# Kernel tuning notes

Measured on AMD Instinct MI355X. Metric: run time of the kernel, lower is better.

The kernel has to match this reference:

```python
import jax, jax.numpy as jnp
import numpy as np

N_NODES = 100000
N_EDGES = 1600000


def setup_inputs() -> dict:
    key = jax.random.key(0)
    ks = jax.random.split(key, 8)
    x = jax.random.normal(ks[0], (N_NODES, 128), dtype=jnp.float32)
    edge_index = jax.random.randint(ks[1], (2, N_EDGES), 0, N_NODES, dtype=jnp.int64)
    # Glorot-ish scaled weights per GCNConv defaults
    W1 = jax.random.normal(ks[2], (128, 64), dtype=jnp.float32) * (1.0 / np.sqrt(128))
    b1 = jnp.zeros((64,), dtype=jnp.float32)
    W2 = jax.random.normal(ks[3], (64, 64), dtype=jnp.float32) * (1.0 / np.sqrt(64))
    b2 = jnp.zeros((64,), dtype=jnp.float32)
    W3 = jax.random.normal(ks[4], (64, 32), dtype=jnp.float32) * (1.0 / np.sqrt(64))
    b3 = jnp.zeros((32,), dtype=jnp.float32)
    return {"x": x, "edge_index": edge_index, "W1": W1, "b1": b1,
            "W2": W2, "b2": b2, "W3": W3, "b3": b3}


def _gcn_norm(edge_index, n_nodes):
    # deg includes self-loop (+1); symmetric normalization D^-1/2 (A+I) D^-1/2
    dst = edge_index[1]
    deg = jax.ops.segment_sum(jnp.ones((edge_index.shape[1],), jnp.float32), dst,
                              num_segments=n_nodes) + 1.0
    dis = jnp.where(deg > 0, jax.lax.rsqrt(deg), 0.0)  # deg_inv_sqrt [N]
    return dis


def _gcn_conv(x, W, b, src, dst, dis, n_nodes):
    h = x @ W                                   # [N, out]
    coef = (dis[src] * dis[dst])[:, None]       # edge norm [E, 1]
    out = jax.ops.segment_sum(h[src] * coef, dst, num_segments=n_nodes)
    out = out + h * (dis * dis)[:, None]        # self-loop contribution
    return out + b


def reference(x, edge_index, W1, b1, W2, b2, W3, b3):
    n = x.shape[0]
    src, dst = edge_index[0], edge_index[1]
    dis = _gcn_norm(edge_index, n)
    h = _gcn_conv(x, W1, b1, src, dst, dis, n)
    h = jax.nn.relu(h)
    h = _gcn_conv(h, W2, b2, src, dst, dis, n)
    h = jax.nn.relu(h)
    h = _gcn_conv(h, W3, b3, src, dst, dis, n)
    return h
```

## Files before the change

kernel.cpp:

```cpp
#include <hip/hip_runtime.h>

#define N_NODES 100000
#define N_EDGES 1600000
#define NB ((N_NODES + 255) >> 8)


__global__ __launch_bounds__(256) void k_bhist(const int* __restrict__ dst,
                                               int* __restrict__ bucket_cnt, int E) {
    __shared__ int h[NB];
    for (int i = threadIdx.x; i < NB; i += 256) h[i] = 0;
    __syncthreads();
    int c0 = blockIdx.x * 4096, c1 = min(c0 + 4096, E);
    for (int i = c0 + threadIdx.x; i < c1; i += 256)
        atomicAdd(&h[dst[i] >> 8], 1);
    __syncthreads();
    for (int i = threadIdx.x; i < NB; i += 256)
        if (h[i]) atomicAdd(&bucket_cnt[i], h[i]);
}

__global__ void k_bscan(const int* __restrict__ bucket_cnt, int* __restrict__ bucket_base,
                        int* __restrict__ bcur, int* __restrict__ row_start) {
    if (threadIdx.x == 0) {
        int run = 0;
        for (int b = 0; b < NB; b++) {
            bucket_base[b] = run; bcur[b] = run; run += bucket_cnt[b];
        }
        bucket_base[NB] = run;
        row_start[N_NODES] = run;
    }
}

__global__ __launch_bounds__(256) void k_partA(const int* __restrict__ src,
                                               const int* __restrict__ dst,
                                               int* __restrict__ bcur,
                                               int2* __restrict__ stage, int E) {
    __shared__ int h[NB];
    __shared__ int cur[NB];
    for (int i = threadIdx.x; i < NB; i += 256) h[i] = 0;
    __syncthreads();
    int c0 = blockIdx.x * 4096, c1 = min(c0 + 4096, E);
    for (int i = c0 + threadIdx.x; i < c1; i += 256)
        atomicAdd(&h[dst[i] >> 8], 1);
    __syncthreads();
    for (int b = threadIdx.x; b < NB; b += 256) {
        int c = h[b];
        cur[b] = c ? atomicAdd(&bcur[b], c) : 0;
    }
    __syncthreads();
    for (int i = c0 + threadIdx.x; i < c1; i += 256) {
        int s = src[i], d = dst[i];
        int pos = atomicAdd(&cur[d >> 8], 1);
        stage[pos] = make_int2(s, d);
    }
}

__global__ __launch_bounds__(256) void k_partB1(const int2* __restrict__ stage,
                                                const int* __restrict__ bucket_base,
                                                int* __restrict__ row_start,
                                                float* __restrict__ dis) {
    __shared__ int cnt[256];
    __shared__ int pref[256];
    int b = blockIdx.x;
    int node0 = b << 8;
    int nn = min(256, N_NODES - node0);
    int t = threadIdx.x;
    cnt[t] = 0;
    __syncthreads();
    int e0 = bucket_base[b], e1 = bucket_base[b + 1];
    for (int e = e0 + t; e < e1; e += 256)
        atomicAdd(&cnt[stage[e].y & 255], 1);
    __syncthreads();
    if (t == 0) {
        int run = e0;
        for (int i = 0; i < nn; i++) { pref[i] = run; run += cnt[i]; }
    }
    __syncthreads();
    if (t < nn) {
        row_start[node0 + t] = pref[t];
        dis[node0 + t] = rsqrtf((float)(cnt[t] + 1));
    }
}

__global__ __launch_bounds__(256) void k_partB2(const int2* __restrict__ stage,
                                                const int* __restrict__ bucket_base,
                                                const int* __restrict__ row_start,
                                                const float* __restrict__ dis,
                                                int2* __restrict__ pairs) {
    __shared__ int cur[256];
    int b = blockIdx.x;
    int node0 = b << 8;
    int nn = min(256, N_NODES - node0);
    int t = threadIdx.x;
    if (t < nn) cur[t] = row_start[node0 + t];
    __syncthreads();
    int e0 = bucket_base[b], e1 = bucket_base[b + 1];
    for (int e = e0 + t; e < e1; e += 256) {
        int2 sd = stage[e];
        float c = dis[sd.x] * dis[sd.y];
        int pos = atomicAdd(&cur[sd.y & 255], 1);
        pairs[pos] = make_int2(sd.x, __float_as_int(c));
    }
}

template <int IN, int OUT>
__global__ __launch_bounds__(256) void k_gemm(const float* __restrict__ A,
                                              const float* __restrict__ W,
                                              float* __restrict__ H, int n) {
    constexpr int BM = 1024 / (OUT / 4);
    __shared__ float Wl[IN * OUT];
    const int tid = threadIdx.x;
    for (int i = tid * 4; i < IN * OUT; i += 1024)
        *(float4*)&Wl[i] = *(const float4*)&W[i];
    __syncthreads();

    const int row0 = blockIdx.x * BM;
    const int tc = tid % (OUT / 4);
    const int tr = tid / (OUT / 4);

    const float* ar[4];
    int row[4];
#pragma unroll
    for (int i = 0; i < 4; i++) {
        row[i] = row0 + tr * 4 + i;
        ar[i] = A + (size_t)min(row[i], n - 1) * IN;
    }

    float4 acc[4];
    acc[0] = acc[1] = acc[2] = acc[3] = make_float4(0.f, 0.f, 0.f, 0.f);

#pragma unroll 4
    for (int k4 = 0; k4 < IN / 4; k4++) {
        float4 av[4], wv[4];
#pragma unroll
        for (int i = 0; i < 4; i++)
            av[i] = *(const float4*)(ar[i] + k4 * 4);
#pragma unroll
        for (int j = 0; j < 4; j++)
            wv[j] = *(float4*)&Wl[(k4 * 4 + j) * OUT + tc * 4];
#pragma unroll
        for (int i = 0; i < 4; i++) {
            acc[i].x += av[i].x * wv[0].x + av[i].y * wv[1].x + av[i].z * wv[2].x + av[i].w * wv[3].x;
            acc[i].y += av[i].x * wv[0].y + av[i].y * wv[1].y + av[i].z * wv[2].y + av[i].w * wv[3].y;
            acc[i].z += av[i].x * wv[0].z + av[i].y * wv[1].z + av[i].z * wv[2].z + av[i].w * wv[3].z;
            acc[i].w += av[i].x * wv[0].w + av[i].y * wv[1].w + av[i].z * wv[2].w + av[i].w * wv[3].w;
        }
    }
#pragma unroll
    for (int i = 0; i < 4; i++)
        if (row[i] < n) *(float4*)&H[(size_t)row[i] * OUT + tc * 4] = acc[i];
}

template <int OUT, bool RELU>
__global__ __launch_bounds__(256) void k_agg(const float* __restrict__ h,
                                             const int2* __restrict__ pairs,
                                             const int* __restrict__ row_start,
                                             const float* __restrict__ dis,
                                             const float* __restrict__ bias,
                                             float* __restrict__ out, int n) {
    constexpr int GROUPS = 256 / OUT;
    constexpr int LPG = OUT / 4;
    int node = (blockIdx.x * blockDim.x + threadIdx.x) >> 6;
    if (node >= n) return;
    int l = threadIdx.x & 63;
    int u = l / LPG;
    int c = (l % LPG) * 4;
    int e0 = row_start[node], e1 = row_start[node + 1];

    float4 acc = make_float4(0.f, 0.f, 0.f, 0.f);
    for (int e = e0; e < e1; e += 2 * GROUPS) {
        int ia = e + u;
        bool va = ia < e1;
        int2 pa = pairs[va ? ia : e0];
        float ca = va ? __int_as_float(pa.y) : 0.f;
        float4 ha = *(const float4*)&h[(size_t)pa.x * OUT + c];
        int ib = e + GROUPS + u;
        bool vb = ib < e1;
        int2 pb = pairs[vb ? ib : e0];
        float cb = vb ? __int_as_float(pb.y) : 0.f;
        float4 hb = *(const float4*)&h[(size_t)pb.x * OUT + c];

        acc.x += ca * ha.x + cb * hb.x;
        acc.y += ca * ha.y + cb * hb.y;
        acc.z += ca * ha.z + cb * hb.z;
        acc.w += ca * ha.w + cb * hb.w;
    }
#pragma unroll
    for (int m = LPG; m < 64; m <<= 1) {
        acc.x += __shfl_xor(acc.x, m);
        acc.y += __shfl_xor(acc.y, m);
        acc.z += __shfl_xor(acc.z, m);
        acc.w += __shfl_xor(acc.w, m);
    }
    if (l < LPG) {
        float dd = dis[node];
        float s = dd * dd;
        float4 hv = *(const float4*)&h[(size_t)node * OUT + c];
        float4 bv = *(const float4*)&bias[c];
        acc.x += s * hv.x + bv.x;
        acc.y += s * hv.y + bv.y;
        acc.z += s * hv.z + bv.z;
        acc.w += s * hv.w + bv.w;
        if (RELU) {
            acc.x = fmaxf(acc.x, 0.f); acc.y = fmaxf(acc.y, 0.f);
            acc.z = fmaxf(acc.z, 0.f); acc.w = fmaxf(acc.w, 0.f);
        }
        *(float4*)&out[(size_t)node * OUT + c] = acc;
    }
}


extern "C" void kernel_launch(void* const* d_in, const int* in_sizes, int n_in,
                              void* d_out, int out_size, void* d_ws, size_t ws_size,
                              hipStream_t stream) {
    const float* x  = (const float*)d_in[0];
    const int*   ei = (const int*)d_in[1];
    const float* W1 = (const float*)d_in[2];
    const float* b1 = (const float*)d_in[3];
    const float* W2 = (const float*)d_in[4];
    const float* b2 = (const float*)d_in[5];
    const float* W3 = (const float*)d_in[6];
    const float* b3 = (const float*)d_in[7];

    char* ws = (char*)d_ws;
    int*   bucket_cnt  = (int*)(ws + 0);
    int*   bucket_base = (int*)(ws + 2048);
    int*   bcur        = (int*)(ws + 4096);
    float* dis         = (float*)(ws + 8192);
    int*   row_start   = (int*)(ws + 408576);
    int2*  pairs       = (int2*)(ws + 809472);
    float* h           = (float*)(ws + 13609472);
    int2*  stage       = (int2*)(ws + 13609472);
    float* a           = (float*)(ws + 39209472);

    const int* src = ei;
    const int* dst = ei + N_EDGES;

    int echunks = (N_EDGES + 4095) / 4096;

    hipMemsetAsync(bucket_cnt, 0, (NB + 1) * sizeof(int), stream);
    k_bhist<<<echunks, 256, 0, stream>>>(dst, bucket_cnt, N_EDGES);
    k_bscan<<<1, 64, 0, stream>>>(bucket_cnt, bucket_base, bcur, row_start);
    k_partA<<<echunks, 256, 0, stream>>>(src, dst, bcur, stage, N_EDGES);
    k_partB1<<<NB, 256, 0, stream>>>(stage, bucket_base, row_start, dis);
    k_partB2<<<NB, 256, 0, stream>>>(stage, bucket_base, row_start, dis, pairs);

    int gemm64 = (N_NODES + 63) / 64;
    int gemm32 = (N_NODES + 127) / 128;
    int aggblk = (N_NODES + 3) / 4;

    k_gemm<128, 64><<<gemm64, 256, 0, stream>>>(x, W1, h, N_NODES);
    k_agg<64, true><<<aggblk, 256, 0, stream>>>(h, pairs, row_start, dis, b1, a, N_NODES);
    k_gemm<64, 64><<<gemm64, 256, 0, stream>>>(a, W2, h, N_NODES);
    k_agg<64, true><<<aggblk, 256, 0, stream>>>(h, pairs, row_start, dis, b2, a, N_NODES);
    k_gemm<64, 32><<<gemm32, 256, 0, stream>>>(a, W3, h, N_NODES);
    k_agg<32, false><<<aggblk, 256, 0, stream>>>(h, pairs, row_start, dis, b3,
                                                 (float*)d_out, N_NODES);
}
```

Measured before the change: 437.3 us.

## Fuse aggregation with following dense transform and prefetch GEMM input rows

Layers 1 and 2 aggregation now apply bias and ReLU and then multiply by the next layer's weight matrix inside the same wavefront, using shuffles and a shared-memory copy of W. This removes two standalone GEMM launches and the write and re-read of the intermediate activations. The remaining GEMM kernel also gets a software prefetch of the next A fragment. In exchange, every aggregation block reloads W into shared memory and performs extra shuffle and LDS work per node.

```diff
diff --git a/kernel.cpp b/kernel.cpp
--- a/kernel.cpp
+++ b/kernel.cpp
@@ -128,12 +128,16 @@
     float4 acc[4];
     acc[0] = acc[1] = acc[2] = acc[3] = make_float4(0.f, 0.f, 0.f, 0.f);
 
+    float4 av[4];
+#pragma unroll
+    for (int i = 0; i < 4; i++) av[i] = *(const float4*)(ar[i]);
+
 #pragma unroll 4
-    for (int k4 = 0; k4 < IN / 4; k4++) {
-        float4 av[4], wv[4];
+    for (int k4 = 0; k4 < IN / 4 - 1; k4++) {
+        float4 nx[4], wv[4];
 #pragma unroll
         for (int i = 0; i < 4; i++)
-            av[i] = *(const float4*)(ar[i] + k4 * 4);
+            nx[i] = *(const float4*)(ar[i] + (k4 + 1) * 4);
 #pragma unroll
         for (int j = 0; j < 4; j++)
             wv[j] = *(float4*)&Wl[(k4 * 4 + j) * OUT + tc * 4];
@@ -144,10 +148,105 @@
             acc[i].z += av[i].x * wv[0].z + av[i].y * wv[1].z + av[i].z * wv[2].z + av[i].w * wv[3].z;
             acc[i].w += av[i].x * wv[0].w + av[i].y * wv[1].w + av[i].z * wv[2].w + av[i].w * wv[3].w;
         }
+#pragma unroll
+        for (int i = 0; i < 4; i++) av[i] = nx[i];
+    }
+    {
+        constexpr int k4 = IN / 4 - 1;
+        float4 wv[4];
+#pragma unroll
+        for (int j = 0; j < 4; j++)
+            wv[j] = *(float4*)&Wl[(k4 * 4 + j) * OUT + tc * 4];
+#pragma unroll
+        for (int i = 0; i < 4; i++) {
+            acc[i].x += av[i].x * wv[0].x + av[i].y * wv[1].x + av[i].z * wv[2].x + av[i].w * wv[3].x;
+            acc[i].y += av[i].x * wv[0].y + av[i].y * wv[1].y + av[i].z * wv[2].y + av[i].w * wv[3].y;
+            acc[i].z += av[i].x * wv[0].z + av[i].y * wv[1].z + av[i].z * wv[2].z + av[i].w * wv[3].z;
+            acc[i].w += av[i].x * wv[0].w + av[i].y * wv[1].w + av[i].z * wv[2].w + av[i].w * wv[3].w;
+        }
     }
 #pragma unroll
     for (int i = 0; i < 4; i++)
         if (row[i] < n) *(float4*)&H[(size_t)row[i] * OUT + tc * 4] = acc[i];
+}
+
+template <int OUT2>
+__global__ __launch_bounds__(256) void k_aggemm(const float* __restrict__ h,
+                                                const int2* __restrict__ pairs,
+                                                const int* __restrict__ row_start,
+                                                const float* __restrict__ dis,
+                                                const float* __restrict__ bias,
+                                                const float* __restrict__ W,
+                                                float* __restrict__ H2, int n) {
+    __shared__ float Wl[64 * OUT2];
+    const int tid = threadIdx.x;
+    for (int i = tid * 4; i < 64 * OUT2; i += 1024)
+        *(float4*)&Wl[i] = *(const float4*)&W[i];
+    __syncthreads();
+
+    int node = (blockIdx.x * blockDim.x + tid) >> 6;
+    if (node >= n) return;
+    int l = tid & 63;
+    int u = l >> 4;
+    int c = (l & 15) * 4;
+    int e0 = row_start[node], e1 = row_start[node + 1];
+
+    float4 acc = make_float4(0.f, 0.f, 0.f, 0.f);
+    for (int e = e0; e < e1; e += 16) {
+#pragma unroll
+        for (int b = 0; b < 4; b++) {
+            int idx = e + b * 4 + u;
+            bool v = idx < e1;
+            int2 p = pairs[v ? idx : e0];
+            float cf = v ? __int_as_float(p.y) : 0.f;
+            float4 hv = *(const float4*)&h[(size_t)p.x * 64 + c];
+            acc.x += cf * hv.x; acc.y += cf * hv.y;
+            acc.z += cf * hv.z; acc.w += cf * hv.w;
+        }
+    }
+#pragma unroll
+    for (int m = 16; m < 64; m <<= 1) {
+        acc.x += __shfl_xor(acc.x, m);
+        acc.y += __shfl_xor(acc.y, m);
+        acc.z += __shfl_xor(acc.z, m);
+        acc.w += __shfl_xor(acc.w, m);
+    }
+    float dd = dis[node];
+    float s = dd * dd;
+    float4 hv = *(const float4*)&h[(size_t)node * 64 + c];
+    float4 bv = *(const float4*)&bias[c];
+    acc.x = fmaxf(acc.x + s * hv.x + bv.x, 0.f);
+    acc.y = fmaxf(acc.y + s * hv.y + bv.y, 0.f);
+    acc.z = fmaxf(acc.z + s * hv.z + bv.z, 0.f);
+    acc.w = fmaxf(acc.w + s * hv.w + bv.w, 0.f);
+
+    if (OUT2 == 64) {
+        float o = 0.f;
+#pragma unroll
+        for (int c16 = 0; c16 < 16; c16++) {
+            float4 v;
+            v.x = __shfl(acc.x, c16); v.y = __shfl(acc.y, c16);
+            v.z = __shfl(acc.z, c16); v.w = __shfl(acc.w, c16);
+            o += v.x * Wl[(4 * c16 + 0) * 64 + l] + v.y * Wl[(4 * c16 + 1) * 64 + l]
+               + v.z * Wl[(4 * c16 + 2) * 64 + l] + v.w * Wl[(4 * c16 + 3) * 64 + l];
+        }
+        H2[(size_t)node * 64 + l] = o;
+    } else {
+        float o = 0.f;
+        int base = (l >> 5) * 8;
+        int col = l & 31;
+#pragma unroll
+        for (int i = 0; i < 8; i++) {
+            int cc = base + i;
+            float4 v;
+            v.x = __shfl(acc.x, cc); v.y = __shfl(acc.y, cc);
+            v.z = __shfl(acc.z, cc); v.w = __shfl(acc.w, cc);
+            o += v.x * Wl[(4 * cc + 0) * 32 + col] + v.y * Wl[(4 * cc + 1) * 32 + col]
+               + v.z * Wl[(4 * cc + 2) * 32 + col] + v.w * Wl[(4 * cc + 3) * 32 + col];
+        }
+        o += __shfl_xor(o, 32);
+        if (l < 32) H2[(size_t)node * 32 + l] = o;
+    }
 }
 
 template <int OUT, bool RELU>
@@ -178,7 +277,6 @@
         int2 pb = pairs[vb ? ib : e0];
         float cb = vb ? __int_as_float(pb.y) : 0.f;
         float4 hb = *(const float4*)&h[(size_t)pb.x * OUT + c];
-
         acc.x += ca * ha.x + cb * hb.x;
         acc.y += ca * ha.y + cb * hb.y;
         acc.z += ca * ha.z + cb * hb.z;
@@ -245,14 +343,11 @@
     k_partB2<<<NB, 256, 0, stream>>>(stage, bucket_base, row_start, dis, pairs);
 
     int gemm64 = (N_NODES + 63) / 64;
-    int gemm32 = (N_NODES + 127) / 128;
     int aggblk = (N_NODES + 3) / 4;
 
     k_gemm<128, 64><<<gemm64, 256, 0, stream>>>(x, W1, h, N_NODES);
-    k_agg<64, true><<<aggblk, 256, 0, stream>>>(h, pairs, row_start, dis, b1, a, N_NODES);
-    k_gemm<64, 64><<<gemm64, 256, 0, stream>>>(a, W2, h, N_NODES);
-    k_agg<64, true><<<aggblk, 256, 0, stream>>>(h, pairs, row_start, dis, b2, a, N_NODES);
-    k_gemm<64, 32><<<gemm32, 256, 0, stream>>>(a, W3, h, N_NODES);
+    k_aggemm<64><<<aggblk, 256, 0, stream>>>(h, pairs, row_start, dis, b1, W2, a, N_NODES);
+    k_aggemm<32><<<aggblk, 256, 0, stream>>>(a, pairs, row_start, dis, b2, W3, h, N_NODES);
     k_agg<32, false><<<aggblk, 256, 0, stream>>>(h, pairs, row_start, dis, b3,
                                                  (float*)d_out, N_NODES);
 }
```

Measured after the change: 463.9 us. 1.06x slower.
